# Kernel optimization log

Hardware: AMD Instinct MI355X
Metric: run time of the kernel (lower is better)

Reference implementation:

```python
import jax, jax.numpy as jnp
import numpy as np

KERNEL_MUL = 2.0
KERNEL_NUM = 5


def _mmd(source, target, kernel_mul=KERNEL_MUL, kernel_num=KERNEL_NUM, fix_sigma=None):
    n = source.shape[0]
    total = jnp.concatenate([source, target], axis=0)  # [2N, D]
    n_samples = total.shape[0]
    # Pairwise squared L2 distances via Gram matrix (same math as the
    # broadcasted (2N,2N,D) diff-square-sum, but O(N^2 D) GEMM instead).
    sq = jnp.sum(total * total, axis=1)                # [2N]
    gram = total @ total.T                             # [2N, 2N]
    L2 = sq[:, None] + sq[None, :] - 2.0 * gram        # [2N, 2N]
    if fix_sigma:
        bandwidth = fix_sigma
    else:
        # torch used L2_distance.data -> detached; match with stop_gradient
        bandwidth = jax.lax.stop_gradient(jnp.sum(L2)) / (n_samples ** 2 - n_samples)
    bandwidth = bandwidth / (kernel_mul ** (kernel_num // 2))
    kernels = jnp.zeros_like(L2)
    for i in range(kernel_num):
        kernels = kernels + jnp.exp(-L2 / (bandwidth * kernel_mul ** i))
    XX = kernels[:n, :n]
    YY = kernels[n:, n:]
    XY = kernels[:n, n:]
    YX = kernels[n:, :n]
    return jnp.mean(XX + YY - XY - YX)


def setup_inputs() -> dict:
    key = jax.random.key(0)
    k1, k2 = jax.random.split(key)
    N, D = 4096, 512
    source = jax.random.normal(k1, (N, D), dtype=jnp.float32)
    target = jax.random.normal(k2, (N, D), dtype=jnp.float32)
    return {"source": source, "target": target}


def reference(source, target):
    # MMD_sample_size = inf >= batch_size -> single full-batch MMD
    return _mmd(source, target)
```

## Files before the change

### kernel.cpp

```cpp
#include <hip/hip_runtime.h>
#include <hip/hip_fp16.h>


#define NS 8192
#define D_DIM 512
#define NTILE 32
#define NBLK 528
#define PBLK 512

typedef _Float16 f16x8 __attribute__((ext_vector_type(8)));
typedef float f32x4 __attribute__((ext_vector_type(4)));

__global__ __launch_bounds__(256) void prep(const float* __restrict__ src,
                                            const float* __restrict__ tgt,
                                            __half* __restrict__ Th,
                                            float* __restrict__ sq,
                                            float* __restrict__ colp,
                                            float* __restrict__ sqp) {
    __shared__ float lcs[4][D_DIM];
    __shared__ float wsq[4];
    int tid = threadIdx.x, w = tid >> 6, l = tid & 63;
    int r0 = blockIdx.x * 16 + w * 4;
    float cs[8];
#pragma unroll
    for (int j = 0; j < 8; ++j) cs[j] = 0.f;
    float ws = 0.f;

#pragma unroll
    for (int rr = 0; rr < 4; ++rr) {
        int r = r0 + rr;
        const float* rowp = (r < 4096) ? (src + (size_t)r * D_DIM)
                                       : (tgt + (size_t)(r - 4096) * D_DIM);
        float4 v0 = *reinterpret_cast<const float4*>(rowp + l * 8);
        float4 v1 = *reinterpret_cast<const float4*>(rowp + l * 8 + 4);
        float f[8] = {v0.x, v0.y, v0.z, v0.w, v1.x, v1.y, v1.z, v1.w};
        __half h[8];
        float s = 0.f;
#pragma unroll
        for (int j = 0; j < 8; ++j) {
            h[j] = __float2half(f[j]);
            float fj = __half2float(h[j]);
            s += fj * fj;
            cs[j] += fj;
        }
        *reinterpret_cast<int4*>(Th + (size_t)r * D_DIM + l * 8) =
            *reinterpret_cast<const int4*>(h);
#pragma unroll
        for (int off = 32; off; off >>= 1) s += __shfl_xor(s, off, 64);
        if (l == 0) { sq[r] = s; ws += s; }
    }
    if (l == 0) wsq[w] = ws;
#pragma unroll
    for (int j = 0; j < 8; ++j) lcs[w][l * 8 + j] = cs[j];
    __syncthreads();
#pragma unroll
    for (int j = 0; j < 2; ++j) {
        int c = j * 256 + tid;
        colp[(size_t)blockIdx.x * D_DIM + c] =
            (lcs[0][c] + lcs[1][c]) + (lcs[2][c] + lcs[3][c]);
    }
    if (tid == 0) sqp[blockIdx.x] = (wsq[0] + wsq[1]) + (wsq[2] + wsq[3]);
}

__global__ __launch_bounds__(512) void combine(const float* __restrict__ colp,
                                               const float* __restrict__ sqp,
                                               float* __restrict__ Sacc,
                                               float* __restrict__ Cacc) {
    __shared__ float red[512];
    __shared__ float red2[512];
    int t = threadIdx.x;
    float s = 0.f;
#pragma unroll 16
    for (int b = 0; b < PBLK; ++b) s += colp[(size_t)b * D_DIM + t];
    float sv = sqp[t];
    red[t] = s * s; red2[t] = sv; __syncthreads();
    for (int off = 256; off; off >>= 1) {
        if (t < off) { red[t] += red[t + off]; red2[t] += red2[t + off]; }
        __syncthreads();
    }
    if (t == 0) { Cacc[0] = red[0]; Sacc[0] = red2[0]; }
}

__global__ __launch_bounds__(512, 2) void mmd_main(const __half* __restrict__ Th,
                                                   const float* __restrict__ sq,
                                                   const float* __restrict__ Sacc,
                                                   const float* __restrict__ Cacc,
                                                   float* __restrict__ partials) {
    __shared__ __half Ah[2][256 * 64];
    __shared__ __half Bh[2][256 * 64];
    __shared__ float wred[8];

    int borig = blockIdx.x;
    int b = (borig & 7) * (NBLK / 8) + (borig >> 3);
    int ti = 0, rem = b;
    while (rem >= NTILE - ti) { rem -= NTILE - ti; ++ti; }
    int tj = ti + rem;
    int ibase = ti * 256, jbase = tj * 256;
    float wgt = ((ti == tj) ? 1.f : 2.f) * (((ti < 16) == (tj < 16)) ? 1.f : -1.f);

    int tid = threadIdx.x;
    int wid = tid >> 6, lane = tid & 63;
    int wm = wid >> 2, wn = wid & 3;
    int cl = lane >> 4;

    double S = (double)Sacc[0];
    double C = (double)Cacc[0];

    f32x4 acc[8][4];
#pragma unroll
    for (int m = 0; m < 8; ++m)
#pragma unroll
        for (int n = 0; n < 4; ++n) acc[m][n] = f32x4{0.f, 0.f, 0.f, 0.f};

    auto STAGE = [&](int buf, int k0) {
#pragma unroll
        for (int it = 0; it < 4; ++it) {
            int h16 = tid + it * 512;
            int row = h16 >> 3, ch = h16 & 7;
            int scol = ((ch ^ (row & 7)) * 8);
            __builtin_amdgcn_global_load_lds(
                (const __attribute__((address_space(1))) unsigned int*)(Th + (size_t)(ibase + row) * D_DIM + k0 + scol),
                (__attribute__((address_space(3))) unsigned int*)(&Ah[buf][h16 * 8]), 16, 0, 0);
            __builtin_amdgcn_global_load_lds(
                (const __attribute__((address_space(1))) unsigned int*)(Th + (size_t)(jbase + row) * D_DIM + k0 + scol),
                (__attribute__((address_space(3))) unsigned int*)(&Bh[buf][h16 * 8]), 16, 0, 0);
        }
    };

    auto COMPUTE = [&](int buf) {
#pragma unroll
        for (int ks = 0; ks < 2; ++ks) {
            f16x8 afr[8], bfr[4];
#pragma unroll
            for (int m = 0; m < 8; ++m) {
                int ra = wm * 128 + m * 16 + (lane & 15);
                int pc = (ks * 4 + cl) ^ (ra & 7);
                afr[m] = *reinterpret_cast<const f16x8*>(&Ah[buf][ra * 64 + pc * 8]);
            }
#pragma unroll
            for (int n = 0; n < 4; ++n) {
                int rb = wn * 64 + n * 16 + (lane & 15);
                int pc = (ks * 4 + cl) ^ (rb & 7);
                bfr[n] = *reinterpret_cast<const f16x8*>(&Bh[buf][rb * 64 + pc * 8]);
            }
#pragma unroll
            for (int m = 0; m < 8; ++m)
#pragma unroll
                for (int n = 0; n < 4; ++n)
                    acc[m][n] = __builtin_amdgcn_mfma_f32_16x16x32_f16(afr[m], bfr[n], acc[m][n], 0, 0, 0);
        }
    };

    STAGE(0, 0);
    __syncthreads();
    int buf = 0;
#pragma unroll
    for (int t = 0; t < 7; ++t) {
        STAGE(buf ^ 1, (t + 1) * 64);
        COMPUTE(buf);
        __syncthreads();
        buf ^= 1;
    }
    COMPUTE(buf);

    double sumL2 = 2.0 * (double)NS * S - 2.0 * C;
    double bwv = sumL2 / ((double)NS * NS - (double)NS) / 4.0;
    float c0s = (float)(-1.4426950408889634 / (bwv * 16.0));
    float m2c0s = -2.f * c0s;

    float sci[32], scj[4];
#pragma unroll
    for (int m = 0; m < 8; ++m)
#pragma unroll
        for (int r = 0; r < 4; ++r)
            sci[m * 4 + r] = sq[ibase + wm * 128 + m * 16 + (lane >> 4) * 4 + r] * c0s;
#pragma unroll
    for (int n = 0; n < 4; ++n)
        scj[n] = sq[jbase + wn * 64 + n * 16 + (lane & 15)] * c0s;

    float ksum = 0.f;
#pragma unroll
    for (int m = 0; m < 8; ++m)
#pragma unroll
        for (int n = 0; n < 4; ++n)
#pragma unroll
            for (int r = 0; r < 4; ++r) {
                float x4 = fmaf(acc[m][n][r], m2c0s, sci[m * 4 + r] + scj[n]);
                float e4 = __builtin_amdgcn_exp2f(x4);
                float e3 = e4 * e4;
                float e2 = e3 * e3;
                float e1 = e2 * e2;
                float e0 = e1 * e1;
                ksum += ((e4 + e3) + (e2 + e1)) + e0;
            }
#pragma unroll
    for (int off = 32; off; off >>= 1) ksum += __shfl_xor(ksum, off, 64);
    if (lane == 0) wred[wid] = ksum;
    __syncthreads();
    if (tid == 0) {
        float tot = ((wred[0] + wred[1]) + (wred[2] + wred[3]))
                  + ((wred[4] + wred[5]) + (wred[6] + wred[7]));
        partials[borig] = tot * wgt;
    }
}

__global__ void finalize(const float* __restrict__ partials, float* __restrict__ out) {
    __shared__ double red[256];
    int t = threadIdx.x;
    double s = 0.0;
    for (int i = t; i < NBLK; i += 256) s += (double)partials[i];
    red[t] = s; __syncthreads();
    for (int off = 128; off; off >>= 1) { if (t < off) red[t] += red[t + off]; __syncthreads(); }
    if (t == 0) out[0] = (float)(red[0] * (1.0 / (4096.0 * 4096.0)));
}

extern "C" void kernel_launch(void* const* d_in, const int* in_sizes, int n_in,
                              void* d_out, int out_size, void* d_ws, size_t ws_size,
                              hipStream_t stream) {
    (void)in_sizes; (void)n_in; (void)out_size; (void)ws_size;
    const float* src = (const float*)d_in[0];
    const float* tgt = (const float*)d_in[1];
    char* ws = (char*)d_ws;
    __half* Th      = (__half*)ws;
    float* sq       = (float*)(ws + 8388608);
    float* colp     = (float*)(ws + 8421376);
    float* sqp      = (float*)(ws + 9469952);
    float* Sacc     = (float*)(ws + 9472000);
    float* Cacc     = (float*)(ws + 9472004);
    float* partials = (float*)(ws + 9472008);
    float* out      = (float*)d_out;

    hipLaunchKernelGGL(prep, dim3(PBLK), dim3(256), 0, stream, src, tgt, Th, sq, colp, sqp);
    hipLaunchKernelGGL(combine, dim3(1), dim3(512), 0, stream, colp, sqp, Sacc, Cacc);
    hipLaunchKernelGGL(mmd_main, dim3(NBLK), dim3(512), 0, stream, Th, sq, Sacc, Cacc, partials);
    hipLaunchKernelGGL(finalize, dim3(1), dim3(256), 0, stream, partials, out);
}
```

Before: 144.5 us.

## Replace combine kernel with atomics and use persistent ticket-scheduled main kernel

Removes the single-block combine kernel. prep now atomically accumulates column sums into 8 replicated buffers and the squared-norm total into one scalar, and mmd_main reduces those replicas itself at startup. mmd_main becomes a persistent kernel with 256 blocks that pull tile indices from an atomic ticket counter, which evens out load across CUs and cuts the tail. The cost is a memset, atomic contention in prep, float-atomic nondeterminism, and the loss of the XCD-aware tile ordering.

```diff
diff --git a/kernel.cpp b/kernel.cpp
--- a/kernel.cpp
+++ b/kernel.cpp
@@ -7,6 +7,7 @@
 #define NTILE 32
 #define NBLK 528
 #define PBLK 512
+#define NREP 8
 
 typedef _Float16 f16x8 __attribute__((ext_vector_type(8)));
 typedef float f32x4 __attribute__((ext_vector_type(4)));
@@ -15,8 +16,8 @@
                                             const float* __restrict__ tgt,
                                             __half* __restrict__ Th,
                                             float* __restrict__ sq,
-                                            float* __restrict__ colp,
-                                            float* __restrict__ sqp) {
+                                            float* __restrict__ colsumR,
+                                            float* __restrict__ Sacc) {
     __shared__ float lcs[4][D_DIM];
     __shared__ float wsq[4];
     int tid = threadIdx.x, w = tid >> 6, l = tid & 63;
@@ -53,66 +54,49 @@
 #pragma unroll
     for (int j = 0; j < 8; ++j) lcs[w][l * 8 + j] = cs[j];
     __syncthreads();
+    float* myrep = colsumR + (blockIdx.x & (NREP - 1)) * D_DIM;
 #pragma unroll
     for (int j = 0; j < 2; ++j) {
         int c = j * 256 + tid;
-        colp[(size_t)blockIdx.x * D_DIM + c] =
-            (lcs[0][c] + lcs[1][c]) + (lcs[2][c] + lcs[3][c]);
+        float v = (lcs[0][c] + lcs[1][c]) + (lcs[2][c] + lcs[3][c]);
+        atomicAdd(&myrep[c], v);
     }
-    if (tid == 0) sqp[blockIdx.x] = (wsq[0] + wsq[1]) + (wsq[2] + wsq[3]);
-}
-
-__global__ __launch_bounds__(512) void combine(const float* __restrict__ colp,
-                                               const float* __restrict__ sqp,
-                                               float* __restrict__ Sacc,
-                                               float* __restrict__ Cacc) {
-    __shared__ float red[512];
-    __shared__ float red2[512];
-    int t = threadIdx.x;
-    float s = 0.f;
-#pragma unroll 16
-    for (int b = 0; b < PBLK; ++b) s += colp[(size_t)b * D_DIM + t];
-    float sv = sqp[t];
-    red[t] = s * s; red2[t] = sv; __syncthreads();
-    for (int off = 256; off; off >>= 1) {
-        if (t < off) { red[t] += red[t + off]; red2[t] += red2[t + off]; }
-        __syncthreads();
-    }
-    if (t == 0) { Cacc[0] = red[0]; Sacc[0] = red2[0]; }
+    if (tid == 0) atomicAdd(Sacc, (wsq[0] + wsq[1]) + (wsq[2] + wsq[3]));
 }
 
 __global__ __launch_bounds__(512, 2) void mmd_main(const __half* __restrict__ Th,
                                                    const float* __restrict__ sq,
+                                                   const float* __restrict__ colsumR,
                                                    const float* __restrict__ Sacc,
-                                                   const float* __restrict__ Cacc,
+                                                   unsigned int* __restrict__ ticket,
                                                    float* __restrict__ partials) {
     __shared__ __half Ah[2][256 * 64];
     __shared__ __half Bh[2][256 * 64];
     __shared__ float wred[8];
-
-    int borig = blockIdx.x;
-    int b = (borig & 7) * (NBLK / 8) + (borig >> 3);
-    int ti = 0, rem = b;
-    while (rem >= NTILE - ti) { rem -= NTILE - ti; ++ti; }
-    int tj = ti + rem;
-    int ibase = ti * 256, jbase = tj * 256;
-    float wgt = ((ti == tj) ? 1.f : 2.f) * (((ti < 16) == (tj < 16)) ? 1.f : -1.f);
+    __shared__ int tIdx;
 
     int tid = threadIdx.x;
     int wid = tid >> 6, lane = tid & 63;
     int wm = wid >> 2, wn = wid & 3;
     int cl = lane >> 4;
 
+    float colv = 0.f;
+#pragma unroll
+    for (int r = 0; r < NREP; ++r) colv += colsumR[r * D_DIM + tid];
+    float c2 = colv * colv;
+#pragma unroll
+    for (int off = 32; off; off >>= 1) c2 += __shfl_xor(c2, off, 64);
+    if (lane == 0) wred[wid] = c2;
+    __syncthreads();
+    float Cf = ((wred[0] + wred[1]) + (wred[2] + wred[3]))
+             + ((wred[4] + wred[5]) + (wred[6] + wred[7]));
     double S = (double)Sacc[0];
-    double C = (double)Cacc[0];
-
-    f32x4 acc[8][4];
-#pragma unroll
-    for (int m = 0; m < 8; ++m)
-#pragma unroll
-        for (int n = 0; n < 4; ++n) acc[m][n] = f32x4{0.f, 0.f, 0.f, 0.f};
-
-    auto STAGE = [&](int buf, int k0) {
+    double sumL2 = 2.0 * (double)NS * S - 2.0 * (double)Cf;
+    double bwv = sumL2 / ((double)NS * NS - (double)NS) / 4.0;
+    float c0s = (float)(-1.4426950408889634 / (bwv * 16.0));
+    float m2c0s = -2.f * c0s;
+
+    auto STAGE = [&](int buf, int ibase, int jbase, int k0) {
 #pragma unroll
         for (int it = 0; it < 4; ++it) {
             int h16 = tid + it * 512;
@@ -127,80 +111,95 @@
         }
     };
 
-    auto COMPUTE = [&](int buf) {
-#pragma unroll
-        for (int ks = 0; ks < 2; ++ks) {
-            f16x8 afr[8], bfr[4];
-#pragma unroll
-            for (int m = 0; m < 8; ++m) {
-                int ra = wm * 128 + m * 16 + (lane & 15);
-                int pc = (ks * 4 + cl) ^ (ra & 7);
-                afr[m] = *reinterpret_cast<const f16x8*>(&Ah[buf][ra * 64 + pc * 8]);
+    for (;;) {
+        __syncthreads();
+        if (tid == 0) tIdx = (int)atomicAdd(ticket, 1u);
+        __syncthreads();
+        int tt = tIdx;
+        if (tt >= NBLK) break;
+
+        int ti = 0, rem = tt;
+        while (rem >= NTILE - ti) { rem -= NTILE - ti; ++ti; }
+        int tj = ti + rem;
+        int ibase = ti * 256, jbase = tj * 256;
+        float wgt = ((ti == tj) ? 1.f : 2.f) * (((ti < 16) == (tj < 16)) ? 1.f : -1.f);
+
+        f32x4 acc[8][4];
+#pragma unroll
+        for (int m = 0; m < 8; ++m)
+#pragma unroll
+            for (int n = 0; n < 4; ++n) acc[m][n] = f32x4{0.f, 0.f, 0.f, 0.f};
+
+        auto COMPUTE = [&](int buf) {
+#pragma unroll
+            for (int ks = 0; ks < 2; ++ks) {
+                f16x8 afr[8], bfr[4];
+#pragma unroll
+                for (int m = 0; m < 8; ++m) {
+                    int ra = wm * 128 + m * 16 + (lane & 15);
+                    int pc = (ks * 4 + cl) ^ (ra & 7);
+                    afr[m] = *reinterpret_cast<const f16x8*>(&Ah[buf][ra * 64 + pc * 8]);
+                }
+#pragma unroll
+                for (int n = 0; n < 4; ++n) {
+                    int rb = wn * 64 + n * 16 + (lane & 15);
+                    int pc = (ks * 4 + cl) ^ (rb & 7);
+                    bfr[n] = *reinterpret_cast<const f16x8*>(&Bh[buf][rb * 64 + pc * 8]);
+                }
+#pragma unroll
+                for (int m = 0; m < 8; ++m)
+#pragma unroll
+                    for (int n = 0; n < 4; ++n)
+                        acc[m][n] = __builtin_amdgcn_mfma_f32_16x16x32_f16(afr[m], bfr[n], acc[m][n], 0, 0, 0);
             }
-#pragma unroll
-            for (int n = 0; n < 4; ++n) {
-                int rb = wn * 64 + n * 16 + (lane & 15);
-                int pc = (ks * 4 + cl) ^ (rb & 7);
-                bfr[n] = *reinterpret_cast<const f16x8*>(&Bh[buf][rb * 64 + pc * 8]);
-            }
-#pragma unroll
-            for (int m = 0; m < 8; ++m)
-#pragma unroll
-                for (int n = 0; n < 4; ++n)
-                    acc[m][n] = __builtin_amdgcn_mfma_f32_16x16x32_f16(afr[m], bfr[n], acc[m][n], 0, 0, 0);
-        }
-    };
-
-    STAGE(0, 0);
-    __syncthreads();
-    int buf = 0;
-#pragma unroll
-    for (int t = 0; t < 7; ++t) {
-        STAGE(buf ^ 1, (t + 1) * 64);
+        };
+
+        STAGE(0, ibase, jbase, 0);
+        __syncthreads();
+        int buf = 0;
+#pragma unroll
+        for (int t = 0; t < 7; ++t) {
+            STAGE(buf ^ 1, ibase, jbase, (t + 1) * 64);
+            COMPUTE(buf);
+            __syncthreads();
+            buf ^= 1;
+        }
         COMPUTE(buf);
-        __syncthreads();
-        buf ^= 1;
-    }
-    COMPUTE(buf);
-
-    double sumL2 = 2.0 * (double)NS * S - 2.0 * C;
-    double bwv = sumL2 / ((double)NS * NS - (double)NS) / 4.0;
-    float c0s = (float)(-1.4426950408889634 / (bwv * 16.0));
-    float m2c0s = -2.f * c0s;
-
-    float sci[32], scj[4];
-#pragma unroll
-    for (int m = 0; m < 8; ++m)
-#pragma unroll
-        for (int r = 0; r < 4; ++r)
-            sci[m * 4 + r] = sq[ibase + wm * 128 + m * 16 + (lane >> 4) * 4 + r] * c0s;
-#pragma unroll
-    for (int n = 0; n < 4; ++n)
-        scj[n] = sq[jbase + wn * 64 + n * 16 + (lane & 15)] * c0s;
-
-    float ksum = 0.f;
-#pragma unroll
-    for (int m = 0; m < 8; ++m)
+
+        float sci[32], scj[4];
+#pragma unroll
+        for (int m = 0; m < 8; ++m)
+#pragma unroll
+            for (int r = 0; r < 4; ++r)
+                sci[m * 4 + r] = sq[ibase + wm * 128 + m * 16 + (lane >> 4) * 4 + r] * c0s;
 #pragma unroll
         for (int n = 0; n < 4; ++n)
-#pragma unroll
-            for (int r = 0; r < 4; ++r) {
-                float x4 = fmaf(acc[m][n][r], m2c0s, sci[m * 4 + r] + scj[n]);
-                float e4 = __builtin_amdgcn_exp2f(x4);
-                float e3 = e4 * e4;
-                float e2 = e3 * e3;
-                float e1 = e2 * e2;
-                float e0 = e1 * e1;
-                ksum += ((e4 + e3) + (e2 + e1)) + e0;
-            }
-#pragma unroll
-    for (int off = 32; off; off >>= 1) ksum += __shfl_xor(ksum, off, 64);
-    if (lane == 0) wred[wid] = ksum;
-    __syncthreads();
-    if (tid == 0) {
-        float tot = ((wred[0] + wred[1]) + (wred[2] + wred[3]))
-                  + ((wred[4] + wred[5]) + (wred[6] + wred[7]));
-        partials[borig] = tot * wgt;
+            scj[n] = sq[jbase + wn * 64 + n * 16 + (lane & 15)] * c0s;
+
+        float ksum = 0.f;
+#pragma unroll
+        for (int m = 0; m < 8; ++m)
+#pragma unroll
+            for (int n = 0; n < 4; ++n)
+#pragma unroll
+                for (int r = 0; r < 4; ++r) {
+                    float x4 = fmaf(acc[m][n][r], m2c0s, sci[m * 4 + r] + scj[n]);
+                    float e4 = __builtin_amdgcn_exp2f(x4);
+                    float e3 = e4 * e4;
+                    float e2 = e3 * e3;
+                    float e1 = e2 * e2;
+                    float e0 = e1 * e1;
+                    ksum += ((e4 + e3) + (e2 + e1)) + e0;
+                }
+#pragma unroll
+        for (int off = 32; off; off >>= 1) ksum += __shfl_xor(ksum, off, 64);
+        if (lane == 0) wred[wid] = ksum;
+        __syncthreads();
+        if (tid == 0) {
+            float tot = ((wred[0] + wred[1]) + (wred[2] + wred[3]))
+                      + ((wred[4] + wred[5]) + (wred[6] + wred[7]));
+            partials[tt] = tot * wgt;
+        }
     }
 }
 
@@ -221,17 +220,16 @@
     const float* src = (const float*)d_in[0];
     const float* tgt = (const float*)d_in[1];
     char* ws = (char*)d_ws;
-    __half* Th      = (__half*)ws;
-    float* sq       = (float*)(ws + 8388608);
-    float* colp     = (float*)(ws + 8421376);
-    float* sqp      = (float*)(ws + 9469952);
-    float* Sacc     = (float*)(ws + 9472000);
-    float* Cacc     = (float*)(ws + 9472004);
-    float* partials = (float*)(ws + 9472008);
-    float* out      = (float*)d_out;
-
-    hipLaunchKernelGGL(prep, dim3(PBLK), dim3(256), 0, stream, src, tgt, Th, sq, colp, sqp);
-    hipLaunchKernelGGL(combine, dim3(1), dim3(512), 0, stream, colp, sqp, Sacc, Cacc);
-    hipLaunchKernelGGL(mmd_main, dim3(NBLK), dim3(512), 0, stream, Th, sq, Sacc, Cacc, partials);
+    __half* Th        = (__half*)ws;
+    float* sq         = (float*)(ws + 8388608);
+    float* colsumR    = (float*)(ws + 8421376);
+    float* Sacc       = (float*)(ws + 8437760);
+    unsigned int* ticket = (unsigned int*)(ws + 8437764);
+    float* partials   = (float*)(ws + 8437768);
+    float* out        = (float*)d_out;
+
+    hipMemsetAsync(colsumR, 0, 16384 + 8, stream);
+    hipLaunchKernelGGL(prep, dim3(PBLK), dim3(256), 0, stream, src, tgt, Th, sq, colsumR, Sacc);
+    hipLaunchKernelGGL(mmd_main, dim3(256), dim3(512), 0, stream, Th, sq, colsumR, Sacc, ticket, partials);
     hipLaunchKernelGGL(finalize, dim3(1), dim3(256), 0, stream, partials, out);
 }
```

New measurement: 140.8 us. 2.6% less time.
